# Kernel optimization log

Hardware: AMD Instinct MI355X
Metric: run time of the kernel (lower is better)

The kernel has to match this reference:

```python
import jax, jax.numpy as jnp
import numpy as np

EMB_W, COMMIT_W, ENT_W = 1.0, 0.25, 0.1  # loss weights from init_kwargs


def setup_inputs() -> dict:
    key = jax.random.key(0)
    k1, k2 = jax.random.split(key)
    B, H, W, D, K = 32, 32, 32, 64, 1024
    inputs = jax.random.normal(k1, (B, H, W, D), dtype=jnp.float32)
    # keras RandomUniform default: U(-0.05, 0.05)
    codebook = jax.random.uniform(k2, (K, D), dtype=jnp.float32, minval=-0.05, maxval=0.05)
    return {"inputs": inputs, "codebook": codebook}


def reference(inputs, codebook):
    # inputs: [B,H,W,D], codebook: [K,D]
    D = inputs.shape[-1]
    x = inputs.reshape(-1, D)  # [N,D]
    dist = (
        jnp.sum(x * x, axis=-1, keepdims=True)
        - 2.0 * (x @ codebook.T)
        + jnp.sum(codebook * codebook, axis=-1)
    )  # [N,K]
    tokens = jnp.argmin(dist, axis=-1)  # [N]
    emb = codebook[tokens].reshape(inputs.shape)  # [B,H,W,D]

    embedding_loss = EMB_W * jnp.mean((jax.lax.stop_gradient(emb) - inputs) ** 2)
    commitment_loss = COMMIT_W * jnp.mean((emb - jax.lax.stop_gradient(inputs)) ** 2)
    # 'entropy' loss as written in call(): mean over codebook of per-code min distance
    entropy_loss = ENT_W * jnp.mean(jnp.min(dist, axis=0))
    loss = embedding_loss + commitment_loss + entropy_loss

    # training=True path: straight-through estimator
    out = inputs + jax.lax.stop_gradient(emb - inputs)
    return out, loss
```

## Files before the change

kernel.cpp:

```cpp
#include <hip/hip_runtime.h>
#include <math.h>

#define NROWS 32768
#define NCODE 1024
#define AMB_CAP 8192
#define GAP_THRESH 1.5e-4f

typedef __attribute__((ext_vector_type(8))) short bf16x8;
typedef __attribute__((ext_vector_type(4))) float f32x4;

__device__ __forceinline__ unsigned short bf16_rne(float f) {
    unsigned u = __float_as_uint(f);
    unsigned r = u + 0x7FFFu + ((u >> 16) & 1u);
    return (unsigned short)(r >> 16);
}

typedef const __attribute__((address_space(1))) unsigned GU;
typedef __attribute__((address_space(3))) unsigned LU;
__device__ __forceinline__ void gl_lds16(const void* g, void* l) {
    __builtin_amdgcn_global_load_lds((GU*)g, (LU*)l, 16, 0, 0);
}
__device__ __forceinline__ void gl_lds4(const void* g, void* l) {
    __builtin_amdgcn_global_load_lds((GU*)g, (LU*)l, 4, 0, 0);
}

__global__ __launch_bounds__(256) void vq_prep(
    const float* __restrict__ cb, float* __restrict__ cn4,
    unsigned* __restrict__ counter, float* __restrict__ gsumsq,
    unsigned* __restrict__ ticket, unsigned short* __restrict__ wsB)
{
    int c = blockIdx.x * 256 + threadIdx.x;
    if (c == 0) { *counter = 0u; *gsumsq = 0.f; *ticket = 0u; }
    if (c >= NCODE) return;
    float v[64];
    const float4* src = (const float4*)(cb + (size_t)c * 64);
    float s = 0.f;
    #pragma unroll
    for (int i = 0; i < 16; i++) {
        float4 t = src[i];
        v[i*4+0] = t.x; v[i*4+1] = t.y; v[i*4+2] = t.z; v[i*4+3] = t.w;
        s += t.x*t.x + t.y*t.y + t.z*t.z + t.w*t.w;
    }
    cn4[c] = s + 4.0f;
    int cc = c >> 6, ct = (c >> 4) & 3, cl = c & 15;
    #pragma unroll
    for (int q = 0; q < 4; q++) {
        int half = q & 1, lo = q >> 1;
        #pragma unroll
        for (int g = 0; g < 4; g++) {
            unsigned short u8[8] __attribute__((aligned(16)));
            #pragma unroll
            for (int j = 0; j < 8; j++) {
                float f = v[half*32 + g*8 + j];
                unsigned short h = bf16_rne(f);
                if (lo) h = bf16_rne(f - __uint_as_float((unsigned)h << 16));
                u8[j] = h;
            }
            size_t off = (size_t)cc * 8192 + ct * 2048 + q * 512 + (g * 16 + cl) * 8;
            *(uint4*)(wsB + off) = *(const uint4*)u8;
        }
    }
}

__global__ __launch_bounds__(256, 4) void vq_main(
    const float* __restrict__ x, const float* __restrict__ cb,
    const unsigned short* __restrict__ wsB, const float* __restrict__ cn4,
    float* __restrict__ out, float* __restrict__ entPartial,
    unsigned* __restrict__ counter, int* __restrict__ amb,
    float* __restrict__ gsumsq)
{
    __shared__ __align__(16) unsigned char Bb[2][16384];
    __shared__ float cn4L[2][64];
    __shared__ unsigned scrE[1024];
    __shared__ int   tokS[64];
    __shared__ float redS[4];

    const int tid = threadIdx.x;
    const int lane = tid & 63;
    const int wi = tid >> 6;
    const int ln15 = lane & 15;
    const int q = lane >> 4;
    const int row0 = blockIdx.x * 64;
    const int wrow = row0 + wi * 16;

    #pragma unroll
    for (int jj = 0; jj < 4; jj++) scrE[jj*256 + tid] = 0x7F800000u;

    const char* wsBb = (const char*)wsB;
    {
        int wbase = (tid & ~63) * 16;
        #pragma unroll
        for (int i = 0; i < 4; i++)
            gl_lds16(wsBb + (i*256 + tid)*16, (void*)&Bb[0][i*4096 + wbase]);
        if (wi == 0) gl_lds4(cn4 + lane, (void*)&cn4L[0][0]);
    }

    bf16x8 Ah0, Ah1, Al0, Al1;
    float xnm4[4];
    {
        const float* xr = x + (size_t)(wrow + ln15) * 64 + q * 8;
        float4 f0 = *(const float4*)xr;
        float4 f1 = *(const float4*)(xr + 4);
        float4 f2 = *(const float4*)(xr + 32);
        float4 f3 = *(const float4*)(xr + 36);
        float fa[8] = {f0.x,f0.y,f0.z,f0.w,f1.x,f1.y,f1.z,f1.w};
        float fb[8] = {f2.x,f2.y,f2.z,f2.w,f3.x,f3.y,f3.z,f3.w};
        unsigned short h[8]  __attribute__((aligned(16)));
        unsigned short l[8]  __attribute__((aligned(16)));
        unsigned short h2[8] __attribute__((aligned(16)));
        unsigned short l2[8] __attribute__((aligned(16)));
        float ss = 0.f;
        #pragma unroll
        for (int j = 0; j < 8; j++) {
            ss += fa[j]*fa[j] + fb[j]*fb[j];
            unsigned short hh = bf16_rne(fa[j]);
            h[j] = hh; l[j] = bf16_rne(fa[j] - __uint_as_float((unsigned)hh << 16));
            hh = bf16_rne(fb[j]);
            h2[j] = hh; l2[j] = bf16_rne(fb[j] - __uint_as_float((unsigned)hh << 16));
        }
        Ah0 = *(const bf16x8*)h;  Al0 = *(const bf16x8*)l;
        Ah1 = *(const bf16x8*)h2; Al1 = *(const bf16x8*)l2;
        ss += __shfl_xor(ss, 16);
        ss += __shfl_xor(ss, 32);
        #pragma unroll
        for (int r = 0; r < 4; r++)
            xnm4[r] = __shfl(ss, (q << 2) | r, 64) - 4.0f;
    }

    float d1[4], d2[4];
    int   i1[4];
    #pragma unroll
    for (int r = 0; r < 4; r++) { d1[r] = INFINITY; d2[r] = INFINITY; i1[r] = 0; }

    for (int cc = 0; cc < 16; cc++) {
        __syncthreads();
        const int cb_ = cc & 1, nb = (cc + 1) & 1;
        if (cc < 15) {
            int wbase = (tid & ~63) * 16;
            #pragma unroll
            for (int i = 0; i < 4; i++)
                gl_lds16(wsBb + (cc+1)*16384 + (i*256 + tid)*16,
                         (void*)&Bb[nb][i*4096 + wbase]);
            if (wi == 0) gl_lds4(cn4 + (cc+1)*64 + lane, (void*)&cn4L[nb][0]);
        }
        const unsigned char* buf = Bb[cb_];
        #pragma unroll
        for (int ct = 0; ct < 4; ct++) {
            bf16x8 Bh0 = *(const bf16x8*)(buf + ct*4096 +    0 + lane*16);
            bf16x8 Bh1 = *(const bf16x8*)(buf + ct*4096 + 1024 + lane*16);
            bf16x8 Bl0 = *(const bf16x8*)(buf + ct*4096 + 2048 + lane*16);
            bf16x8 Bl1 = *(const bf16x8*)(buf + ct*4096 + 3072 + lane*16);
            float cn4v = cn4L[cb_][ct*16 + ln15];
            int kid = cc*64 + ct*16 + ln15;
            f32x4 acc = {0.f, 0.f, 0.f, 0.f};
            acc = __builtin_amdgcn_mfma_f32_16x16x32_bf16(Ah0, Bh0, acc, 0, 0, 0);
            acc = __builtin_amdgcn_mfma_f32_16x16x32_bf16(Ah1, Bh1, acc, 0, 0, 0);
            acc = __builtin_amdgcn_mfma_f32_16x16x32_bf16(Ah0, Bl0, acc, 0, 0, 0);
            acc = __builtin_amdgcn_mfma_f32_16x16x32_bf16(Ah1, Bl1, acc, 0, 0, 0);
            acc = __builtin_amdgcn_mfma_f32_16x16x32_bf16(Al0, Bh0, acc, 0, 0, 0);
            acc = __builtin_amdgcn_mfma_f32_16x16x32_bf16(Al1, Bh1, acc, 0, 0, 0);
            float cminv = INFINITY;
            #pragma unroll
            for (int r = 0; r < 4; r++) {
                float wv = fmaf(acc[r], -2.0f, cn4v);
                bool lt = wv < d1[r];
                d2[r] = lt ? d1[r] : fminf(d2[r], wv);
                i1[r] = lt ? kid   : i1[r];
                d1[r] = lt ? wv    : d1[r];
                cminv = fminf(cminv, wv + xnm4[r]);
            }
            cminv = fminf(cminv, __shfl_xor(cminv, 16));
            cminv = fminf(cminv, __shfl_xor(cminv, 32));
            if (q == ct) atomicMin(&scrE[kid], __float_as_uint(cminv));
        }
    }
    __syncthreads();

    #pragma unroll
    for (int d = 1; d < 16; d <<= 1) {
        #pragma unroll
        for (int r = 0; r < 4; r++) {
            float od1 = __shfl_xor(d1[r], d);
            int   oi1 = __shfl_xor(i1[r], d);
            float od2 = __shfl_xor(d2[r], d);
            bool take = (od1 < d1[r]) || (od1 == d1[r] && oi1 < i1[r]);
            float loser = take ? d1[r] : od1;
            d2[r] = fminf(fminf(d2[r], od2), loser);
            d1[r] = take ? od1 : d1[r];
            i1[r] = take ? oi1 : i1[r];
        }
    }
    if (ln15 == 0) {
        #pragma unroll
        for (int r = 0; r < 4; r++) {
            tokS[wi*16 + q*4 + r] = i1[r];
            if (d2[r] - d1[r] < GAP_THRESH) {
                unsigned idx = atomicAdd(counter, 1u);
                if (idx < AMB_CAP) {
                    amb[2*idx]   = row0 + wi*16 + q*4 + r;
                    amb[2*idx+1] = i1[r];
                }
            }
        }
    }
    __syncthreads();

    #pragma unroll
    for (int jj = 0; jj < 4; jj++) {
        int c = jj*256 + tid;
        entPartial[(size_t)blockIdx.x * 1024 + c] = __uint_as_float(scrE[c]);
    }

    {
        int grow = tid >> 2, p = tid & 3;
        int tok = tokS[grow];
        const float4* cv = (const float4*)(cb + (size_t)tok*64 + p*16);
        const float4* xv = (const float4*)(x  + (size_t)(row0 + grow)*64 + p*16);
        float4* ov = (float4*)(out + (size_t)(row0 + grow)*64 + p*16);
        float acc2 = 0.f;
        #pragma unroll
        for (int i = 0; i < 4; i++) {
            float4 c = cv[i]; float4 xx = xv[i];
            ov[i] = c;
            float dx = c.x-xx.x, dy = c.y-xx.y, dz = c.z-xx.z, dw = c.w-xx.w;
            acc2 += dx*dx + dy*dy + dz*dz + dw*dw;
        }
        #pragma unroll
        for (int o = 32; o > 0; o >>= 1) acc2 += __shfl_down(acc2, o);
        if ((tid & 63) == 0) redS[tid >> 6] = acc2;
        __syncthreads();
        if (tid == 0) atomicAdd(gsumsq, redS[0] + redS[1] + redS[2] + redS[3]);
    }
}

__global__ __launch_bounds__(256) void vq_tail(
    const float* __restrict__ x, const float* __restrict__ cb,
    float* __restrict__ out, const float* __restrict__ entPartial,
    const unsigned* __restrict__ counter, const int* __restrict__ amb,
    float* __restrict__ gsumsq, unsigned* __restrict__ ticket,
    float* __restrict__ minDist, float* __restrict__ out_loss)
{
    __shared__ double xs[64];
    __shared__ double bd[256];
    __shared__ int    bi[256];
    __shared__ unsigned lastS;
    __shared__ float redS[4];

    const int tid = threadIdx.x;
    const int lane = tid & 63;

    {
        int code = blockIdx.x * 4 + (tid >> 6);
        const float* p = entPartial + (size_t)lane * 1024 + code;
        float m = INFINITY;
        #pragma unroll
        for (int j = 0; j < 8; j++) m = fminf(m, p[(size_t)j * 64 * 1024]);
        #pragma unroll
        for (int o = 32; o > 0; o >>= 1) m = fminf(m, __shfl_down(m, o));
        if (lane == 0) minDist[code] = m;
    }

    unsigned cnt = *counter; if (cnt > AMB_CAP) cnt = AMB_CAP;
    for (unsigned i = blockIdx.x; i < cnt; i += gridDim.x) {
        int row = amb[2*i], oldk = amb[2*i+1];
        __syncthreads();
        if (tid < 64) xs[tid] = (double)x[(size_t)row*64 + tid];
        __syncthreads();
        double xn = 0.0;
        #pragma unroll 8
        for (int d = 0; d < 64; d++) xn += xs[d]*xs[d];
        double best = INFINITY; int bk = 1 << 30;
        #pragma unroll
        for (int j = 0; j < 4; j++) {
            int k = j*256 + tid;
            const float4* c4 = (const float4*)(cb + (size_t)k*64);
            double dot = 0.0, cn2 = 0.0;
            #pragma unroll
            for (int t = 0; t < 16; t++) {
                float4 cv = c4[t];
                double cx = (double)cv.x, cy = (double)cv.y, cz = (double)cv.z, cw = (double)cv.w;
                dot += xs[t*4+0]*cx + xs[t*4+1]*cy + xs[t*4+2]*cz + xs[t*4+3]*cw;
                cn2 += cx*cx + cy*cy + cz*cz + cw*cw;
            }
            double dist = (xn - 2.0*dot) + cn2;
            if (dist < best || (dist == best && k < bk)) { best = dist; bk = k; }
        }
        bd[tid] = best; bi[tid] = bk;
        __syncthreads();
        for (int s = 128; s > 0; s >>= 1) {
            if (tid < s) {
                double od = bd[tid+s]; int ok = bi[tid+s];
                if (od < bd[tid] || (od == bd[tid] && ok < bi[tid])) { bd[tid] = od; bi[tid] = ok; }
            }
            __syncthreads();
        }
        int bestk = bi[0];
        if (bestk != oldk) {
            double part = 0.0;
            if (tid < 64) {
                float cn = cb[(size_t)bestk*64 + tid];
                float co = cb[(size_t)oldk*64 + tid];
                out[(size_t)row*64 + tid] = cn;
                double dn = (double)cn - xs[tid];
                double dl = (double)co - xs[tid];
                part = dn*dn - dl*dl;
            }
            __syncthreads();
            bd[tid] = part;
            __syncthreads();
            for (int s = 128; s > 0; s >>= 1) {
                if (tid < s) bd[tid] += bd[tid+s];
                __syncthreads();
            }
            if (tid == 0) atomicAdd(gsumsq, (float)bd[0]);
        }
    }

    __syncthreads();
    if (tid == 0) {
        __threadfence();
        lastS = (atomicAdd(ticket, 1u) == (unsigned)(gridDim.x - 1)) ? 1u : 0u;
    }
    __syncthreads();
    if (lastS) {
        __threadfence();
        volatile const float* md = minDist;
        float s = 0.f;
        #pragma unroll
        for (int jj = 0; jj < 4; jj++) s += md[jj*256 + tid];
        #pragma unroll
        for (int o = 32; o > 0; o >>= 1) s += __shfl_down(s, o);
        if ((tid & 63) == 0) redS[tid >> 6] = s;
        __syncthreads();
        if (tid == 0) {
            volatile const float* gs = gsumsq;
            float tot = redS[0] + redS[1] + redS[2] + redS[3];
            out_loss[0] = 1.25f * (*gs / 2097152.0f) + 0.1f * (tot / 1024.0f);
        }
    }
}

extern "C" void kernel_launch(void* const* d_in, const int* in_sizes, int n_in,
                              void* d_out, int out_size, void* d_ws, size_t ws_size,
                              hipStream_t stream) {
    const float* x  = (const float*)d_in[0];
    const float* cb = (const float*)d_in[1];
    float* out = (float*)d_out;

    char* ws = (char*)d_ws;
    unsigned*       counter    = (unsigned*)ws;
    float*          gsumsq     = (float*)(ws + 4);
    unsigned*       ticket     = (unsigned*)(ws + 8);
    float*          cn4        = (float*)(ws + 1024);
    int*            amb        = (int*)(ws + 16384);
    unsigned short* wsB        = (unsigned short*)(ws + 131072);
    float*          minDist    = (float*)(ws + 393216);
    float*          entPartial = (float*)(ws + 524288);

    vq_prep<<<4,   256, 0, stream>>>(cb, cn4, counter, gsumsq, ticket, wsB);
    vq_main<<<512, 256, 0, stream>>>(x, cb, wsB, cn4, out, entPartial, counter, amb, gsumsq);
    vq_tail<<<256, 256, 0, stream>>>(x, cb, out, entPartial, counter, amb, gsumsq, ticket,
                                     minDist, out + 2097152);
}
```

Measured before the change: 138.9 us.

## Reduce per-code min distance with global atomicMin and rotate codebook chunk order

Each vq_main block now folds its per-code min distances into a global minK array with atomicMin on the float bit patterns, valid because they are non-negative. This replaces the 2 MB entPartial write and the partial-reduction pass in vq_tail. Blocks also start at a codebook chunk rotated by block index, which spreads L2 and atomic traffic across chunks. vq_tail shrinks to 64 blocks, adding atomic contention on 1024 addresses and leaving fewer blocks for the ambiguous-row fixup.

```diff
diff --git a/kernel.cpp b/kernel.cpp
--- a/kernel.cpp
+++ b/kernel.cpp
@@ -26,8 +26,9 @@
 
 __global__ __launch_bounds__(256) void vq_prep(
     const float* __restrict__ cb, float* __restrict__ cn4,
-    unsigned* __restrict__ counter, float* __restrict__ gsumsq,
-    unsigned* __restrict__ ticket, unsigned short* __restrict__ wsB)
+    unsigned* __restrict__ minK, unsigned* __restrict__ counter,
+    float* __restrict__ gsumsq, unsigned* __restrict__ ticket,
+    unsigned short* __restrict__ wsB)
 {
     int c = blockIdx.x * 256 + threadIdx.x;
     if (c == 0) { *counter = 0u; *gsumsq = 0.f; *ticket = 0u; }
@@ -42,6 +43,7 @@
         s += t.x*t.x + t.y*t.y + t.z*t.z + t.w*t.w;
     }
     cn4[c] = s + 4.0f;
+    minK[c] = 0x7F800000u;
     int cc = c >> 6, ct = (c >> 4) & 3, cl = c & 15;
     #pragma unroll
     for (int q = 0; q < 4; q++) {
@@ -65,7 +67,7 @@
 __global__ __launch_bounds__(256, 4) void vq_main(
     const float* __restrict__ x, const float* __restrict__ cb,
     const unsigned short* __restrict__ wsB, const float* __restrict__ cn4,
-    float* __restrict__ out, float* __restrict__ entPartial,
+    float* __restrict__ out, unsigned* __restrict__ minK,
     unsigned* __restrict__ counter, int* __restrict__ amb,
     float* __restrict__ gsumsq)
 {
@@ -81,7 +83,7 @@
     const int ln15 = lane & 15;
     const int q = lane >> 4;
     const int row0 = blockIdx.x * 64;
-    const int wrow = row0 + wi * 16;
+    const int rot = blockIdx.x & 15;
 
     #pragma unroll
     for (int jj = 0; jj < 4; jj++) scrE[jj*256 + tid] = 0x7F800000u;
@@ -91,14 +93,14 @@
         int wbase = (tid & ~63) * 16;
         #pragma unroll
         for (int i = 0; i < 4; i++)
-            gl_lds16(wsBb + (i*256 + tid)*16, (void*)&Bb[0][i*4096 + wbase]);
-        if (wi == 0) gl_lds4(cn4 + lane, (void*)&cn4L[0][0]);
+            gl_lds16(wsBb + rot*16384 + (i*256 + tid)*16, (void*)&Bb[0][i*4096 + wbase]);
+        if (wi == 0) gl_lds4(cn4 + rot*64 + lane, (void*)&cn4L[0][0]);
     }
 
     bf16x8 Ah0, Ah1, Al0, Al1;
     float xnm4[4];
     {
-        const float* xr = x + (size_t)(wrow + ln15) * 64 + q * 8;
+        const float* xr = x + (size_t)(row0 + wi*16 + ln15) * 64 + q * 8;
         float4 f0 = *(const float4*)xr;
         float4 f1 = *(const float4*)(xr + 4);
         float4 f2 = *(const float4*)(xr + 32);
@@ -132,16 +134,18 @@
     #pragma unroll
     for (int r = 0; r < 4; r++) { d1[r] = INFINITY; d2[r] = INFINITY; i1[r] = 0; }
 
-    for (int cc = 0; cc < 16; cc++) {
-        __syncthreads();
-        const int cb_ = cc & 1, nb = (cc + 1) & 1;
-        if (cc < 15) {
+    for (int s = 0; s < 16; s++) {
+        __syncthreads();
+        const int cb_ = s & 1, nb = (s + 1) & 1;
+        const int cphys = (s + rot) & 15;
+        if (s < 15) {
+            const int cnx = (s + 1 + rot) & 15;
             int wbase = (tid & ~63) * 16;
             #pragma unroll
             for (int i = 0; i < 4; i++)
-                gl_lds16(wsBb + (cc+1)*16384 + (i*256 + tid)*16,
+                gl_lds16(wsBb + cnx*16384 + (i*256 + tid)*16,
                          (void*)&Bb[nb][i*4096 + wbase]);
-            if (wi == 0) gl_lds4(cn4 + (cc+1)*64 + lane, (void*)&cn4L[nb][0]);
+            if (wi == 0) gl_lds4(cn4 + cnx*64 + lane, (void*)&cn4L[nb][0]);
         }
         const unsigned char* buf = Bb[cb_];
         #pragma unroll
@@ -151,7 +155,7 @@
             bf16x8 Bl0 = *(const bf16x8*)(buf + ct*4096 + 2048 + lane*16);
             bf16x8 Bl1 = *(const bf16x8*)(buf + ct*4096 + 3072 + lane*16);
             float cn4v = cn4L[cb_][ct*16 + ln15];
-            int kid = cc*64 + ct*16 + ln15;
+            int kid = cphys*64 + ct*16 + ln15;
             f32x4 acc = {0.f, 0.f, 0.f, 0.f};
             acc = __builtin_amdgcn_mfma_f32_16x16x32_bf16(Ah0, Bh0, acc, 0, 0, 0);
             acc = __builtin_amdgcn_mfma_f32_16x16x32_bf16(Ah1, Bh1, acc, 0, 0, 0);
@@ -208,7 +212,8 @@
     #pragma unroll
     for (int jj = 0; jj < 4; jj++) {
         int c = jj*256 + tid;
-        entPartial[(size_t)blockIdx.x * 1024 + c] = __uint_as_float(scrE[c]);
+        unsigned u = scrE[c];
+        if (u < minK[c]) atomicMin(&minK[c], u);
     }
 
     {
@@ -235,10 +240,10 @@
 
 __global__ __launch_bounds__(256) void vq_tail(
     const float* __restrict__ x, const float* __restrict__ cb,
-    float* __restrict__ out, const float* __restrict__ entPartial,
-    const unsigned* __restrict__ counter, const int* __restrict__ amb,
-    float* __restrict__ gsumsq, unsigned* __restrict__ ticket,
-    float* __restrict__ minDist, float* __restrict__ out_loss)
+    float* __restrict__ out, const unsigned* __restrict__ counter,
+    const int* __restrict__ amb, float* __restrict__ gsumsq,
+    unsigned* __restrict__ ticket, const unsigned* __restrict__ minK,
+    float* __restrict__ out_loss)
 {
     __shared__ double xs[64];
     __shared__ double bd[256];
@@ -247,18 +252,6 @@
     __shared__ float redS[4];
 
     const int tid = threadIdx.x;
-    const int lane = tid & 63;
-
-    {
-        int code = blockIdx.x * 4 + (tid >> 6);
-        const float* p = entPartial + (size_t)lane * 1024 + code;
-        float m = INFINITY;
-        #pragma unroll
-        for (int j = 0; j < 8; j++) m = fminf(m, p[(size_t)j * 64 * 1024]);
-        #pragma unroll
-        for (int o = 32; o > 0; o >>= 1) m = fminf(m, __shfl_down(m, o));
-        if (lane == 0) minDist[code] = m;
-    }
 
     unsigned cnt = *counter; if (cnt > AMB_CAP) cnt = AMB_CAP;
     for (unsigned i = blockIdx.x; i < cnt; i += gridDim.x) {
@@ -324,18 +317,18 @@
     __syncthreads();
     if (lastS) {
         __threadfence();
-        volatile const float* md = minDist;
         float s = 0.f;
         #pragma unroll
-        for (int jj = 0; jj < 4; jj++) s += md[jj*256 + tid];
+        for (int jj = 0; jj < 4; jj++)
+            s += __uint_as_float(minK[jj*256 + tid]);
         #pragma unroll
         for (int o = 32; o > 0; o >>= 1) s += __shfl_down(s, o);
         if ((tid & 63) == 0) redS[tid >> 6] = s;
         __syncthreads();
         if (tid == 0) {
-            volatile const float* gs = gsumsq;
+            float gs = atomicAdd(gsumsq, 0.0f);
             float tot = redS[0] + redS[1] + redS[2] + redS[3];
-            out_loss[0] = 1.25f * (*gs / 2097152.0f) + 0.1f * (tot / 1024.0f);
+            out_loss[0] = 1.25f * (gs / 2097152.0f) + 0.1f * (tot / 1024.0f);
         }
     }
 }
@@ -348,17 +341,16 @@
     float* out = (float*)d_out;
 
     char* ws = (char*)d_ws;
-    unsigned*       counter    = (unsigned*)ws;
-    float*          gsumsq     = (float*)(ws + 4);
-    unsigned*       ticket     = (unsigned*)(ws + 8);
-    float*          cn4        = (float*)(ws + 1024);
-    int*            amb        = (int*)(ws + 16384);
-    unsigned short* wsB        = (unsigned short*)(ws + 131072);
-    float*          minDist    = (float*)(ws + 393216);
-    float*          entPartial = (float*)(ws + 524288);
-
-    vq_prep<<<4,   256, 0, stream>>>(cb, cn4, counter, gsumsq, ticket, wsB);
-    vq_main<<<512, 256, 0, stream>>>(x, cb, wsB, cn4, out, entPartial, counter, amb, gsumsq);
-    vq_tail<<<256, 256, 0, stream>>>(x, cb, out, entPartial, counter, amb, gsumsq, ticket,
-                                     minDist, out + 2097152);
-}
+    unsigned*       counter = (unsigned*)ws;
+    float*          gsumsq  = (float*)(ws + 4);
+    unsigned*       ticket  = (unsigned*)(ws + 8);
+    float*          cn4     = (float*)(ws + 1024);
+    unsigned*       minK    = (unsigned*)(ws + 8192);
+    int*            amb     = (int*)(ws + 16384);
+    unsigned short* wsB     = (unsigned short*)(ws + 131072);
+
+    vq_prep<<<4,   256, 0, stream>>>(cb, cn4, minK, counter, gsumsq, ticket, wsB);
+    vq_main<<<512, 256, 0, stream>>>(x, cb, wsB, cn4, out, minK, counter, amb, gsumsq);
+    vq_tail<<<64,  256, 0, stream>>>(x, cb, out, counter, amb, gsumsq, ticket, minK,
+                                     out + 2097152);
+}
```

Measured after the change: 136.2 us. 2.0% less time.
